# Optimization experiments

Hardware: AMD Instinct MI355X
Metric: run time of the kernel (lower is better)

## Reference

```python
import jax, jax.numpy as jnp
import numpy as np

# norse LIFParameters defaults: tau_syn_inv=200, tau_mem_inv=100, v_leak=0, v_th=1, v_reset=0
DT = 0.001
TAU_SYN_INV = 200.0
TAU_MEM_INV = 100.0
V_TH = 1.0
ALPHA = 100.0  # super-spike surrogate slope

@jax.custom_vjp
def spike(x):
    return (x > 0).astype(x.dtype)

def _spike_fwd(x):
    return (x > 0).astype(x.dtype), x

def _spike_bwd(x, g):
    return (g / (ALPHA * jnp.abs(x) + 1.0) ** 2,)

spike.defvjp(_spike_fwd, _spike_bwd)

def setup_inputs() -> dict:
    key = jax.random.key(0)
    ks = jax.random.split(key, 5)
    T, B, C, FS = 100, 256, 3, 32
    H, D, O, NOUT = 200, 3, 4, 10
    K = H // O
    x = jax.random.normal(ks[0], (T, B, C, FS, FS), dtype=jnp.float32)
    # 3 input channels x 3 dendritic sub-cells, each Linear(FS*FS -> H)
    W_h = jax.random.normal(ks[1], (C, D, H, FS * FS), dtype=jnp.float32) * 0.03
    b_h = jax.random.normal(ks[2], (C, D, H), dtype=jnp.float32) * 0.01
    # 4 output branches, each Linear(K -> 10) feeding a leaky integrator
    W_o = jax.random.normal(ks[3], (O, NOUT, K), dtype=jnp.float32) * 0.1
    b_o = jax.random.normal(ks[4], (O, NOUT), dtype=jnp.float32) * 0.01
    return {"x": x, "W_h": W_h, "b_h": b_h, "W_o": W_o, "b_o": b_o}

def reference(x, W_h, b_h, W_o, b_o):
    T, B = x.shape[0], x.shape[1]
    C, D, H = W_h.shape[0], W_h.shape[1], W_h.shape[2]
    O, NOUT, K = W_o.shape
    xf = x.reshape(T, B, C, -1)  # flatten(1) of each channel slice
    vh0 = jnp.zeros((C, D, B, H), x.dtype)
    ih0 = jnp.zeros((C, D, B, H), x.dtype)
    vo0 = jnp.zeros((O, B, NOUT), x.dtype)
    io0 = jnp.zeros((O, B, NOUT), x.dtype)

    def step(state, x_t):
        vh, ih, vo, io = state
        # hidden dendritic LIF cells (norse lif_feed_forward_step order)
        vh_dec = vh + DT * TAU_MEM_INV * (-vh + ih)  # v_leak = 0
        ih_dec = ih * (1.0 - DT * TAU_SYN_INV)
        zh = spike(vh_dec - V_TH)                    # (C, D, B, H)
        vh_new = (1.0 - zh) * vh_dec                 # v_reset = 0
        inj = jnp.einsum('bci,cdhi->cdbh', x_t, W_h) + b_h[:, :, None, :]
        ih_new = ih_dec + inj
        z = zh.sum(axis=(0, 1))                      # summed dendritic spikes (B, H)
        # output: O contiguous chunks of z -> leaky-integrator readouts
        zs = z.reshape(B, O, K).transpose(1, 0, 2)   # (O, B, K)
        vo_new = vo + DT * TAU_MEM_INV * (-vo + io)
        io_new = io * (1.0 - DT * TAU_SYN_INV) \
                 + jnp.einsum('obk,onk->obn', zs, W_o) + b_o[:, None, :]
        v = vo_new.sum(axis=0)                       # (B, 10)
        return (vh_new, ih_new, vo_new, io_new), v

    _, voltages = jax.lax.scan(step, (vh0, ih0, vo0, io0), xf)
    return voltages  # (T, B, 10)
```

## Files before the change

kernel.cpp:

```cpp
#include <hip/hip_runtime.h>
#include <stdint.h>

#define TOTAL_T 100
#define NB 256
#define NH 200
#define NJ (NB*NH)
#define KDIM 1024
#define NEFF 600
#define NPAD 640
#define NTILES 5
#define KBLKS 32

#define BM 128
#define BN 128
#define AST 1040

#define WCHUNK 4096
#define NWHALF (3 * KBLKS * NTILES * WCHUNK)

typedef _Float16 f16x8 __attribute__((ext_vector_type(8)));
typedef float    f32x4 __attribute__((ext_vector_type(4)));

__global__ __launch_bounds__(256) void presplit_wh(
    const float* __restrict__ Wh, unsigned short* __restrict__ WH,
    unsigned short* __restrict__ WM)
{
    int idx = blockIdx.x * 256 + threadIdx.x;
    if (idx >= 3 * NPAD * KDIM) return;
    int k = idx & (KDIM - 1);
    int n = (idx >> 10) % NPAD;
    int c = idx / (NPAD * KDIM);
    float v = 0.f;
    if (n < NEFF) v = Wh[((size_t)c * NEFF + n) * KDIM + k];
    _Float16 h = (_Float16)v;
    float r = v - (float)h;
    _Float16 m = (_Float16)r;
    int kb = k >> 5, kg = (k >> 3) & 3, kj = k & 7;
    int nt = n >> 7, row = n & 127;
    size_t off = (((size_t)c * KBLKS + kb) * NTILES + nt) * WCHUNK
               + (kg * 128 + row) * 8 + kj;
    WH[off] = __builtin_bit_cast(unsigned short, h);
    WM[off] = __builtin_bit_cast(unsigned short, m);
}

#define SPLIT_A()                                                               \
  {                                                                             \
    _Pragma("unroll")                                                           \
    for (int l = 0; l < 4; ++l) {                                               \
      int row_ = srow + (l << 5);                                               \
      float a0 = av[l].x, a1 = av[l].y, a2 = av[l].z, a3 = av[l].w;             \
      _Float16 h0 = (_Float16)a0, h1 = (_Float16)a1,                            \
               h2 = (_Float16)a2, h3 = (_Float16)a3;                            \
      _Float16 q0 = (_Float16)(a0 - (float)h0), q1 = (_Float16)(a1 - (float)h1),\
               q2 = (_Float16)(a2 - (float)h2), q3 = (_Float16)(a3 - (float)h3);\
      uint32_t hw0 = (uint32_t)__builtin_bit_cast(unsigned short, h0)           \
                   | ((uint32_t)__builtin_bit_cast(unsigned short, h1) << 16);  \
      uint32_t hw1 = (uint32_t)__builtin_bit_cast(unsigned short, h2)           \
                   | ((uint32_t)__builtin_bit_cast(unsigned short, h3) << 16);  \
      uint32_t mw0 = (uint32_t)__builtin_bit_cast(unsigned short, q0)           \
                   | ((uint32_t)__builtin_bit_cast(unsigned short, q1) << 16);  \
      uint32_t mw1 = (uint32_t)__builtin_bit_cast(unsigned short, q2)           \
                   | ((uint32_t)__builtin_bit_cast(unsigned short, q3) << 16);  \
      int off_ = kgw * AST + row_ * 8 + kjw;                                    \
      *reinterpret_cast<uint2*>(&Ah[off_]) = make_uint2(hw0, hw1);              \
      *reinterpret_cast<uint2*>(&Am[off_]) = make_uint2(mw0, mw1);              \
    }                                                                           \
  }

#define GEMM_ITER(KB, BCH, BCM, BNH, BNM)                                       \
  {                                                                             \
    const int kb_ = (KB);                                                       \
    if (kb_ + 1 < KBLKS) {                                                      \
      const unsigned short* nbh_ = bhp + (size_t)(kb_ + 1) * (NTILES * WCHUNK); \
      const unsigned short* nbm_ = bmp + (size_t)(kb_ + 1) * (NTILES * WCHUNK); \
      _Pragma("unroll")                                                         \
      for (int ni = 0; ni < 4; ++ni) {                                          \
        BNH[ni] = *reinterpret_cast<const f16x8*>(nbh_ + bfroff + (ni << 7));   \
        BNM[ni] = *reinterpret_cast<const f16x8*>(nbm_ + bfroff + (ni << 7));   \
      }                                                                         \
      _Pragma("unroll")                                                         \
      for (int l = 0; l < 4; ++l)                                               \
        av[l] = *reinterpret_cast<const float4*>(                               \
            xb + (size_t)(srow + (l << 5)) * 3 * KDIM + ((kb_ + 1) << 5));      \
    }                                                                           \
    f16x8 afh[4], afm[4];                                                       \
    _Pragma("unroll")                                                           \
    for (int mi = 0; mi < 4; ++mi) {                                            \
      int aoff_ = kg * AST + (mbase + (mi << 4) + lrow) * 8;                    \
      afh[mi] = *reinterpret_cast<const f16x8*>(&Ah[aoff_]);                    \
      afm[mi] = *reinterpret_cast<const f16x8*>(&Am[aoff_]);                    \
    }                                                                           \
    asm volatile("s_waitcnt lgkmcnt(0)" ::: "memory");                          \
    __builtin_amdgcn_s_barrier();                                               \
    __builtin_amdgcn_sched_barrier(0);                                          \
    __builtin_amdgcn_s_setprio(1);                                              \
    _Pragma("unroll")                                                           \
    for (int ni = 0; ni < 4; ++ni)                                              \
      _Pragma("unroll")                                                         \
      for (int mi = 0; mi < 4; ++mi) {                                          \
        f32x4 a_ = acc[mi][ni];                                                 \
        a_ = __builtin_amdgcn_mfma_f32_16x16x32_f16(afh[mi], BCH[ni], a_,0,0,0);\
        a_ = __builtin_amdgcn_mfma_f32_16x16x32_f16(afh[mi], BCM[ni], a_,0,0,0);\
        a_ = __builtin_amdgcn_mfma_f32_16x16x32_f16(afm[mi], BCH[ni], a_,0,0,0);\
        acc[mi][ni] = a_;                                                       \
      }                                                                         \
    __builtin_amdgcn_s_setprio(0);                                              \
    __builtin_amdgcn_sched_barrier(0);                                          \
    if (kb_ + 1 < KBLKS) { SPLIT_A(); }                                         \
    asm volatile("s_waitcnt lgkmcnt(0)" ::: "memory");                          \
    __builtin_amdgcn_s_barrier();                                               \
    __builtin_amdgcn_sched_barrier(0);                                          \
  }

__global__ __launch_bounds__(256, 2) void gemm_inj_mfma(
    const float* __restrict__ x,
    const unsigned short* __restrict__ WH,
    const unsigned short* __restrict__ WM,
    const float* __restrict__ bh,
    float* __restrict__ inj,
    int Mc, int MBlk)
{
    __shared__ __align__(16) unsigned short Ah[4 * AST], Am[4 * AST];

    const int tid  = threadIdx.x;
    const int lane = tid & 63;
    const int w    = tid >> 6;
    const int mbase = (w >> 1) * 64;
    const int nbase = (w & 1) * 64;

    const int nblk = gridDim.x;
    const int hwid = blockIdx.x;
    const int xcd  = hwid & 7, jj = hwid >> 3;
    const int q = nblk >> 3, rr = nblk & 7;
    const int L = (xcd < rr ? xcd * (q + 1) : rr * (q + 1) + (xcd - rr) * q) + jj;
    const int c   = L / (NTILES * MBlk);
    const int rem = L - c * (NTILES * MBlk);
    const int mb  = rem / NTILES;
    const int nt  = rem - mb * NTILES;
    const int n0 = nt * BN;
    const int m0 = mb * BM;

    f32x4 acc[4][4];
#pragma unroll
    for (int i = 0; i < 4; ++i)
#pragma unroll
        for (int j = 0; j < 4; ++j) acc[i][j] = (f32x4)0.f;

    const int srow = tid >> 3;
    const int skq  = (tid & 7) << 2;
    const int kgw  = skq >> 3;
    const int kjw  = skq & 7;
    const int kg   = lane >> 4;
    const int lrow = lane & 15;
    const int bfroff = ((kg << 7) + nbase + lrow) << 3;

    const unsigned short* bhp = WH + ((size_t)c * KBLKS * NTILES + nt) * WCHUNK;
    const unsigned short* bmp = WM + ((size_t)c * KBLKS * NTILES + nt) * WCHUNK;
    const float* xb = x + (size_t)m0 * 3 * KDIM + (size_t)c * KDIM + skq;

    f16x8 bAh[4], bAm[4], bBh[4], bBm[4];
    float4 av[4];

#pragma unroll
    for (int ni = 0; ni < 4; ++ni) {
        bAh[ni] = *reinterpret_cast<const f16x8*>(bhp + bfroff + (ni << 7));
        bAm[ni] = *reinterpret_cast<const f16x8*>(bmp + bfroff + (ni << 7));
    }
#pragma unroll
    for (int l = 0; l < 4; ++l)
        av[l] = *reinterpret_cast<const float4*>(xb + (size_t)(srow + (l << 5)) * 3 * KDIM);
    SPLIT_A();
    asm volatile("s_waitcnt lgkmcnt(0)" ::: "memory");
    __builtin_amdgcn_s_barrier();
    __builtin_amdgcn_sched_barrier(0);

    for (int kb2 = 0; kb2 < KBLKS; kb2 += 2) {
        GEMM_ITER(kb2,     bAh, bAm, bBh, bBm);
        GEMM_ITER(kb2 + 1, bBh, bBm, bAh, bAm);
    }

#pragma unroll
    for (int ni = 0; ni < 4; ++ni) {
        int ncol = n0 + nbase + (ni << 4) + lrow;
        if (ncol >= NEFF) continue;
        int d = ncol / 200;
        int h = ncol - d * 200;
        float bias = bh[c * NEFF + ncol];
        size_t obase = (size_t)(c * 3 + d) * Mc;
#pragma unroll
        for (int mi = 0; mi < 4; ++mi) {
            int mrow = m0 + mbase + (mi << 4) + ((lane >> 4) << 2);
#pragma unroll
            for (int r = 0; r < 4; ++r)
                inj[(obase + mrow + r) * NH + h] = acc[mi][ni][r] + bias;
        }
    }
}

__global__ __launch_bounds__(256) void scan_z(
    const float* __restrict__ inj,
    float* __restrict__ z,
    float* __restrict__ vhs, float* __restrict__ ihs,
    int Tc, int first)
{
    int j = blockIdx.x * 256 + threadIdx.x;
    float vh[9], ih[9];
    if (first) {
#pragma unroll
        for (int cd = 0; cd < 9; ++cd) { vh[cd] = 0.f; ih[cd] = 0.f; }
    } else {
#pragma unroll
        for (int cd = 0; cd < 9; ++cd) {
            vh[cd] = vhs[cd * NJ + j];
            ih[cd] = ihs[cd * NJ + j];
        }
    }
    float ivc[9], ivn[9];
#pragma unroll
    for (int cd = 0; cd < 9; ++cd)
        ivc[cd] = inj[(size_t)cd * Tc * NJ + j];
    if (Tc > 1) {
#pragma unroll
        for (int cd = 0; cd < 9; ++cd)
            ivn[cd] = inj[((size_t)cd * Tc + 1) * NJ + j];
    }
    for (int t = 0; t < Tc; ++t) {
        float zs = 0.f;
#pragma unroll
        for (int cd = 0; cd < 9; ++cd) {
            float iv = ivc[cd];
            ivc[cd] = ivn[cd];
            float vd = vh[cd] + 0.1f * (ih[cd] - vh[cd]);
            ih[cd] = 0.8f * ih[cd] + iv;
            if (vd > 1.0f) { zs += 1.f; vh[cd] = 0.f; }
            else           { vh[cd] = vd; }
        }
        z[(size_t)t * NJ + j] = zs;
        if (t + 2 < Tc) {
#pragma unroll
            for (int cd = 0; cd < 9; ++cd)
                ivn[cd] = inj[((size_t)cd * Tc + t + 2) * NJ + j];
        }
    }
#pragma unroll
    for (int cd = 0; cd < 9; ++cd) {
        vhs[cd * NJ + j] = vh[cd];
        ihs[cd * NJ + j] = ih[cd];
    }
}

__global__ __launch_bounds__(256) void readout(
    const float* __restrict__ z,
    const float* __restrict__ Wo,
    const float* __restrict__ bo,
    float* __restrict__ out,
    float* __restrict__ ios, float* __restrict__ vos,
    int t0, int Tc, int first)
{
    const int b = blockIdx.x;
    const int tid = threadIdx.x;
    __shared__ float ush[TOTAL_T][40];
    __shared__ float usum[TOTAL_T][10];
    __shared__ float p9[TOTAL_T + 1], p8[TOTAL_T + 1];
    __shared__ float wsh[2000], bsh[40];
    for (int i = tid; i < 2000; i += 256) wsh[i] = Wo[i];
    if (tid < 40) bsh[tid] = bo[tid];
    if (tid == 0) {
        float a9 = 1.f, a8 = 1.f;
        for (int i = 0; i <= TOTAL_T; ++i) {
            p9[i] = a9; p8[i] = a8; a9 *= 0.9f; a8 *= 0.8f;
        }
    }
    __syncthreads();
    for (int it = tid; it < Tc * 40; it += 256) {
        int s = it / 40, on = it - s * 40;
        int o = on / 10;
        const float* zr = z + (size_t)s * NJ + b * NH + o * 50;
        const float* wr = &wsh[on * 50];
        float dot = bsh[on];
#pragma unroll
        for (int k = 0; k < 50; ++k) dot += zr[k] * wr[k];
        ush[s][on] = dot;
    }
    __syncthreads();
    for (int it = tid; it < Tc * 10; it += 256) {
        int s = it / 10, n = it - s * 10;
        usum[s][n] = ush[s][n] + ush[s][10 + n] + ush[s][20 + n] + ush[s][30 + n];
    }
    __syncthreads();
    for (int it = tid; it < Tc * 10; it += 256) {
        int t = it / 10, n = it - t * 10;
        float a = 0.f;
        for (int s = 0; s <= t; ++s)
            a += (p9[t - s] - p8[t - s]) * usum[s][n];
        if (!first) {
#pragma unroll
            for (int o = 0; o < 4; ++o) {
                int on = o * 10 + n;
                a += p9[t + 1] * vos[b * 40 + on]
                   + (p9[t + 1] - p8[t + 1]) * ios[b * 40 + on];
            }
        }
        out[((size_t)(t0 + t) * NB + b) * 10 + n] = a;
    }
    __syncthreads();
    if (tid < 40) {
        int on = tid;
        float io0 = 0.f, vo0 = 0.f;
        if (!first) { io0 = ios[b * 40 + on]; vo0 = vos[b * 40 + on]; }
        float sio = 0.f, svo = 0.f;
        for (int s = 0; s < Tc; ++s) {
            sio += p8[Tc - 1 - s] * ush[s][on];
            svo += (p9[Tc - 1 - s] - p8[Tc - 1 - s]) * ush[s][on];
        }
        ios[b * 40 + on] = p8[Tc] * io0 + sio;
        vos[b * 40 + on] = p9[Tc] * vo0 + (p9[Tc] - p8[Tc]) * io0 + svo;
    }
}

extern "C" void kernel_launch(void* const* d_in, const int* in_sizes, int n_in,
                              void* d_out, int out_size, void* d_ws, size_t ws_size,
                              hipStream_t stream) {
    (void)in_sizes; (void)n_in; (void)out_size;
    const float* x  = (const float*)d_in[0];
    const float* Wh = (const float*)d_in[1];
    const float* bh = (const float*)d_in[2];
    const float* Wo = (const float*)d_in[3];
    const float* bo = (const float*)d_in[4];
    float* out = (float*)d_out;

    float* vhs  = (float*)d_ws;
    float* ihs  = vhs + 9 * NJ;
    float* ios  = ihs + 9 * NJ;
    float* vos  = ios + NB * 40;
    unsigned short* WHl = (unsigned short*)(vos + NB * 40);
    unsigned short* WMl = WHl + NWHALF;
    float* inj  = (float*)(WMl + NWHALF);

    size_t fixed = ((size_t)9 * NJ * 2 + (size_t)NB * 40 * 2) * 4
                 + (size_t)NWHALF * 2 * 2;
    size_t per_t = (size_t)NB * (9 * NH * 4 + NH * 4);
    int Tc = 1;
    for (int t = TOTAL_T; t >= 1; --t) {
        if (fixed + (size_t)t * per_t <= ws_size) { Tc = t; break; }
    }

    presplit_wh<<<(3 * NPAD * KDIM + 255) / 256, 256, 0, stream>>>(Wh, WHl, WMl);

    for (int t0 = 0; t0 < TOTAL_T; t0 += Tc) {
        int tc = (TOTAL_T - t0 < Tc) ? (TOTAL_T - t0) : Tc;
        int Mc = tc * NB;
        int MBlk = Mc / BM;
        float* zbuf = inj + (size_t)9 * Mc * NH;
        gemm_inj_mfma<<<NTILES * MBlk * 3, 256, 0, stream>>>(
            x + (size_t)t0 * NB * 3 * KDIM, WHl, WMl, bh, inj, Mc, MBlk);
        scan_z<<<NJ / 256, 256, 0, stream>>>(inj, zbuf, vhs, ihs, tc, t0 == 0);
        readout<<<NB, 256, 0, stream>>>(
            zbuf, Wo, bo, out, ios, vos, t0, tc, t0 == 0);
    }
}
```

Before: 450.6 us.

## Load A fragments directly into registers, dropping LDS staging and barriers

The A tile is no longer staged through shared memory. Each lane now loads the eight fp32 values of its own MFMA fragment straight from global memory and splits them into fp16 high and low parts in registers. This removes the LDS writes and reads and both workgroup barriers per K step, with the A and B loads for the next K block software-pipelined around the MFMA cluster. The block-index decomposition also changes so blocks sharing the same N tile run consecutively, which should improve B-weight cache reuse. In exchange, the two waves covering the same rows issue duplicate global loads of x, and there is less slack to hide global latency than with the LDS buffer.

```diff
diff --git a/kernel.cpp b/kernel.cpp
--- a/kernel.cpp
+++ b/kernel.cpp
@@ -13,7 +13,6 @@
 
 #define BM 128
 #define BN 128
-#define AST 1040
 
 #define WCHUNK 4096
 #define NWHALF (3 * KBLKS * NTILES * WCHUNK)
@@ -43,73 +42,56 @@
     WM[off] = __builtin_bit_cast(unsigned short, m);
 }
 
-#define SPLIT_A()                                                               \
+
+#define LOAD_AB(KB, BH_, BM_)                                                   \
   {                                                                             \
     _Pragma("unroll")                                                           \
-    for (int l = 0; l < 4; ++l) {                                               \
-      int row_ = srow + (l << 5);                                               \
-      float a0 = av[l].x, a1 = av[l].y, a2 = av[l].z, a3 = av[l].w;             \
-      _Float16 h0 = (_Float16)a0, h1 = (_Float16)a1,                            \
-               h2 = (_Float16)a2, h3 = (_Float16)a3;                            \
-      _Float16 q0 = (_Float16)(a0 - (float)h0), q1 = (_Float16)(a1 - (float)h1),\
-               q2 = (_Float16)(a2 - (float)h2), q3 = (_Float16)(a3 - (float)h3);\
-      uint32_t hw0 = (uint32_t)__builtin_bit_cast(unsigned short, h0)           \
-                   | ((uint32_t)__builtin_bit_cast(unsigned short, h1) << 16);  \
-      uint32_t hw1 = (uint32_t)__builtin_bit_cast(unsigned short, h2)           \
-                   | ((uint32_t)__builtin_bit_cast(unsigned short, h3) << 16);  \
-      uint32_t mw0 = (uint32_t)__builtin_bit_cast(unsigned short, q0)           \
-                   | ((uint32_t)__builtin_bit_cast(unsigned short, q1) << 16);  \
-      uint32_t mw1 = (uint32_t)__builtin_bit_cast(unsigned short, q2)           \
-                   | ((uint32_t)__builtin_bit_cast(unsigned short, q3) << 16);  \
-      int off_ = kgw * AST + row_ * 8 + kjw;                                    \
-      *reinterpret_cast<uint2*>(&Ah[off_]) = make_uint2(hw0, hw1);              \
-      *reinterpret_cast<uint2*>(&Am[off_]) = make_uint2(mw0, mw1);              \
+    for (int mi = 0; mi < 4; ++mi) {                                            \
+      avn[2 * mi]     = *reinterpret_cast<const float4*>(ap[mi] + ((KB) << 5));     \
+      avn[2 * mi + 1] = *reinterpret_cast<const float4*>(ap[mi] + ((KB) << 5) + 4); \
+    }                                                                           \
+    const unsigned short* nb_ = bhp + (size_t)(KB) * (NTILES * WCHUNK);         \
+    const unsigned short* nm_ = bmp + (size_t)(KB) * (NTILES * WCHUNK);         \
+    _Pragma("unroll")                                                           \
+    for (int ni = 0; ni < 4; ++ni) {                                            \
+      BH_[ni] = *reinterpret_cast<const f16x8*>(nb_ + (ni << 7));               \
+      BM_[ni] = *reinterpret_cast<const f16x8*>(nm_ + (ni << 7));               \
     }                                                                           \
   }
 
-#define GEMM_ITER(KB, BCH, BCM, BNH, BNM)                                       \
+#define SPLIT_AV()                                                              \
   {                                                                             \
-    const int kb_ = (KB);                                                       \
-    if (kb_ + 1 < KBLKS) {                                                      \
-      const unsigned short* nbh_ = bhp + (size_t)(kb_ + 1) * (NTILES * WCHUNK); \
-      const unsigned short* nbm_ = bmp + (size_t)(kb_ + 1) * (NTILES * WCHUNK); \
-      _Pragma("unroll")                                                         \
-      for (int ni = 0; ni < 4; ++ni) {                                          \
-        BNH[ni] = *reinterpret_cast<const f16x8*>(nbh_ + bfroff + (ni << 7));   \
-        BNM[ni] = *reinterpret_cast<const f16x8*>(nbm_ + bfroff + (ni << 7));   \
-      }                                                                         \
-      _Pragma("unroll")                                                         \
-      for (int l = 0; l < 4; ++l)                                               \
-        av[l] = *reinterpret_cast<const float4*>(                               \
-            xb + (size_t)(srow + (l << 5)) * 3 * KDIM + ((kb_ + 1) << 5));      \
-    }                                                                           \
-    f16x8 afh[4], afm[4];                                                       \
     _Pragma("unroll")                                                           \
     for (int mi = 0; mi < 4; ++mi) {                                            \
-      int aoff_ = kg * AST + (mbase + (mi << 4) + lrow) * 8;                    \
-      afh[mi] = *reinterpret_cast<const f16x8*>(&Ah[aoff_]);                    \
-      afm[mi] = *reinterpret_cast<const f16x8*>(&Am[aoff_]);                    \
+      float xr[8];                                                              \
+      xr[0] = avn[2 * mi].x;     xr[1] = avn[2 * mi].y;                         \
+      xr[2] = avn[2 * mi].z;     xr[3] = avn[2 * mi].w;                         \
+      xr[4] = avn[2 * mi + 1].x; xr[5] = avn[2 * mi + 1].y;                     \
+      xr[6] = avn[2 * mi + 1].z; xr[7] = avn[2 * mi + 1].w;                     \
+      _Pragma("unroll")                                                         \
+      for (int j2 = 0; j2 < 8; ++j2) {                                          \
+        _Float16 hv = (_Float16)xr[j2];                                         \
+        _Float16 mv = (_Float16)(xr[j2] - (float)hv);                           \
+        afh[mi][j2] = hv;                                                       \
+        afm[mi][j2] = mv;                                                       \
+      }                                                                         \
     }                                                                           \
-    asm volatile("s_waitcnt lgkmcnt(0)" ::: "memory");                          \
-    __builtin_amdgcn_s_barrier();                                               \
-    __builtin_amdgcn_sched_barrier(0);                                          \
+  }
+
+#define MFMA_CL(BH_, BM_)                                                       \
+  {                                                                             \
     __builtin_amdgcn_s_setprio(1);                                              \
     _Pragma("unroll")                                                           \
     for (int ni = 0; ni < 4; ++ni)                                              \
       _Pragma("unroll")                                                         \
       for (int mi = 0; mi < 4; ++mi) {                                          \
         f32x4 a_ = acc[mi][ni];                                                 \
-        a_ = __builtin_amdgcn_mfma_f32_16x16x32_f16(afh[mi], BCH[ni], a_,0,0,0);\
-        a_ = __builtin_amdgcn_mfma_f32_16x16x32_f16(afh[mi], BCM[ni], a_,0,0,0);\
-        a_ = __builtin_amdgcn_mfma_f32_16x16x32_f16(afm[mi], BCH[ni], a_,0,0,0);\
+        a_ = __builtin_amdgcn_mfma_f32_16x16x32_f16(afh[mi], BH_[ni], a_,0,0,0);\
+        a_ = __builtin_amdgcn_mfma_f32_16x16x32_f16(afh[mi], BM_[ni], a_,0,0,0);\
+        a_ = __builtin_amdgcn_mfma_f32_16x16x32_f16(afm[mi], BH_[ni], a_,0,0,0);\
         acc[mi][ni] = a_;                                                       \
       }                                                                         \
     __builtin_amdgcn_s_setprio(0);                                              \
-    __builtin_amdgcn_sched_barrier(0);                                          \
-    if (kb_ + 1 < KBLKS) { SPLIT_A(); }                                         \
-    asm volatile("s_waitcnt lgkmcnt(0)" ::: "memory");                          \
-    __builtin_amdgcn_s_barrier();                                               \
-    __builtin_amdgcn_sched_barrier(0);                                          \
   }
 
 __global__ __launch_bounds__(256, 2) void gemm_inj_mfma(
@@ -120,8 +102,6 @@
     float* __restrict__ inj,
     int Mc, int MBlk)
 {
-    __shared__ __align__(16) unsigned short Ah[4 * AST], Am[4 * AST];
-
     const int tid  = threadIdx.x;
     const int lane = tid & 63;
     const int w    = tid >> 6;
@@ -135,49 +115,56 @@
     const int L = (xcd < rr ? xcd * (q + 1) : rr * (q + 1) + (xcd - rr) * q) + jj;
     const int c   = L / (NTILES * MBlk);
     const int rem = L - c * (NTILES * MBlk);
-    const int mb  = rem / NTILES;
-    const int nt  = rem - mb * NTILES;
+    const int nt  = rem / MBlk;
+    const int mb  = rem - nt * MBlk;
     const int n0 = nt * BN;
     const int m0 = mb * BM;
 
-    f32x4 acc[4][4];
-#pragma unroll
-    for (int i = 0; i < 4; ++i)
-#pragma unroll
-        for (int j = 0; j < 4; ++j) acc[i][j] = (f32x4)0.f;
-
-    const int srow = tid >> 3;
-    const int skq  = (tid & 7) << 2;
-    const int kgw  = skq >> 3;
-    const int kjw  = skq & 7;
     const int kg   = lane >> 4;
     const int lrow = lane & 15;
     const int bfroff = ((kg << 7) + nbase + lrow) << 3;
 
-    const unsigned short* bhp = WH + ((size_t)c * KBLKS * NTILES + nt) * WCHUNK;
-    const unsigned short* bmp = WM + ((size_t)c * KBLKS * NTILES + nt) * WCHUNK;
-    const float* xb = x + (size_t)m0 * 3 * KDIM + (size_t)c * KDIM + skq;
-
-    f16x8 bAh[4], bAm[4], bBh[4], bBm[4];
-    float4 av[4];
-
-#pragma unroll
-    for (int ni = 0; ni < 4; ++ni) {
-        bAh[ni] = *reinterpret_cast<const f16x8*>(bhp + bfroff + (ni << 7));
-        bAm[ni] = *reinterpret_cast<const f16x8*>(bmp + bfroff + (ni << 7));
-    }
-#pragma unroll
-    for (int l = 0; l < 4; ++l)
-        av[l] = *reinterpret_cast<const float4*>(xb + (size_t)(srow + (l << 5)) * 3 * KDIM);
-    SPLIT_A();
-    asm volatile("s_waitcnt lgkmcnt(0)" ::: "memory");
-    __builtin_amdgcn_s_barrier();
+    f32x4 acc[4][4];
+#pragma unroll
+    for (int i = 0; i < 4; ++i)
+#pragma unroll
+        for (int j = 0; j < 4; ++j) acc[i][j] = (f32x4)0.f;
+
+    const float* ap[4];
+#pragma unroll
+    for (int mi = 0; mi < 4; ++mi)
+        ap[mi] = x + (size_t)(m0 + mbase + (mi << 4) + lrow) * (3 * KDIM)
+               + (size_t)c * KDIM + (kg << 3);
+
+    const unsigned short* bhp = WH + ((size_t)c * KBLKS * NTILES + nt) * WCHUNK + bfroff;
+    const unsigned short* bmp = WM + ((size_t)c * KBLKS * NTILES + nt) * WCHUNK + bfroff;
+
+    float4 avn[8];
+    f16x8 b0h[4], b0m[4], b1h[4], b1m[4];
+    f16x8 afh[4], afm[4];
+
+    LOAD_AB(0, b0h, b0m);
+    SPLIT_AV();
+
+    for (int kb2 = 0; kb2 < KBLKS - 2; kb2 += 2) {
+        LOAD_AB(kb2 + 1, b1h, b1m);
+        __builtin_amdgcn_sched_barrier(0);
+        MFMA_CL(b0h, b0m);
+        __builtin_amdgcn_sched_barrier(0);
+        SPLIT_AV();
+        LOAD_AB(kb2 + 2, b0h, b0m);
+        __builtin_amdgcn_sched_barrier(0);
+        MFMA_CL(b1h, b1m);
+        __builtin_amdgcn_sched_barrier(0);
+        SPLIT_AV();
+    }
+    LOAD_AB(KBLKS - 1, b1h, b1m);
     __builtin_amdgcn_sched_barrier(0);
-
-    for (int kb2 = 0; kb2 < KBLKS; kb2 += 2) {
-        GEMM_ITER(kb2,     bAh, bAm, bBh, bBm);
-        GEMM_ITER(kb2 + 1, bBh, bBm, bAh, bAm);
-    }
+    MFMA_CL(b0h, b0m);
+    __builtin_amdgcn_sched_barrier(0);
+    SPLIT_AV();
+    __builtin_amdgcn_sched_barrier(0);
+    MFMA_CL(b1h, b1m);
 
 #pragma unroll
     for (int ni = 0; ni < 4; ++ni) {
```

Result: slower. 682.0 us (+51.4%).

## Stage B operand through triple-buffered LDS via async global_load_lds

Applied to the files above, without the earlier changes.

The precomputed fp16 hi/lo weight tiles are no longer loaded from global memory straight into registers per wave. They are now copied with global_load_lds into a three-deep LDS ring buffer, prefetched two K-blocks ahead, and read into fragments from LDS. The goal is to hide global-memory latency behind the MFMA work and to stop each wave from fetching its own B fragments separately. The cost is 48KB of extra LDS per block, which could limit occupancy, plus hand-tuned vmcnt waits whose counts must match the issued loads exactly. The K loop is reorganised into a 3-way unrolled main loop plus a peeled two-block epilogue.

```diff
diff --git a/kernel.cpp b/kernel.cpp
--- a/kernel.cpp
+++ b/kernel.cpp
@@ -20,6 +20,8 @@
 
 typedef _Float16 f16x8 __attribute__((ext_vector_type(8)));
 typedef float    f32x4 __attribute__((ext_vector_type(4)));
+typedef __attribute__((address_space(3))) uint32_t as3_u32;
+typedef __attribute__((address_space(1))) uint32_t as1_u32;
 
 __global__ __launch_bounds__(256) void presplit_wh(
     const float* __restrict__ Wh, unsigned short* __restrict__ WH,
@@ -43,16 +45,41 @@
     WM[off] = __builtin_bit_cast(unsigned short, m);
 }
 
+
+#define LOAD_A(KB)                                                              \
+  {                                                                             \
+    _Pragma("unroll")                                                           \
+    for (int l = 0; l < 4; ++l)                                                 \
+      avn[l] = *reinterpret_cast<const float4*>(                                \
+          xb + (size_t)(srow + (l << 5)) * 3 * KDIM + ((KB) << 5));             \
+  }
+
+#define DMA_B(KB, BUF)                                                          \
+  {                                                                             \
+    const unsigned short* nbh_ = bhp + (size_t)(KB) * (NTILES * WCHUNK);        \
+    const unsigned short* nbm_ = bmp + (size_t)(KB) * (NTILES * WCHUNK);        \
+    _Pragma("unroll")                                                           \
+    for (int i = 0; i < 2; ++i) {                                               \
+      int seg = (i << 2) + w;                                                   \
+      __builtin_amdgcn_global_load_lds(                                         \
+          (const as1_u32*)(nbh_ + ((seg << 6) + lane) * 8),                     \
+          (as3_u32*)&Bh[BUF][seg << 9], 16, 0, 0);                              \
+      __builtin_amdgcn_global_load_lds(                                         \
+          (const as1_u32*)(nbm_ + ((seg << 6) + lane) * 8),                     \
+          (as3_u32*)&Bm[BUF][seg << 9], 16, 0, 0);                              \
+    }                                                                           \
+  }
+
 #define SPLIT_A()                                                               \
   {                                                                             \
     _Pragma("unroll")                                                           \
     for (int l = 0; l < 4; ++l) {                                               \
       int row_ = srow + (l << 5);                                               \
-      float a0 = av[l].x, a1 = av[l].y, a2 = av[l].z, a3 = av[l].w;             \
+      float a0 = avn[l].x, a1 = avn[l].y, a2 = avn[l].z, a3 = avn[l].w;         \
       _Float16 h0 = (_Float16)a0, h1 = (_Float16)a1,                            \
                h2 = (_Float16)a2, h3 = (_Float16)a3;                            \
-      _Float16 q0 = (_Float16)(a0 - (float)h0), q1 = (_Float16)(a1 - (float)h1),\
-               q2 = (_Float16)(a2 - (float)h2), q3 = (_Float16)(a3 - (float)h3);\
+      _Float16 q0 = (_Float16)(a0 - (float)h0), q1 = (_Float16)(a1 - (float)h1);\
+      _Float16 q2 = (_Float16)(a2 - (float)h2), q3 = (_Float16)(a3 - (float)h3);\
       uint32_t hw0 = (uint32_t)__builtin_bit_cast(unsigned short, h0)           \
                    | ((uint32_t)__builtin_bit_cast(unsigned short, h1) << 16);  \
       uint32_t hw1 = (uint32_t)__builtin_bit_cast(unsigned short, h2)           \
@@ -67,46 +94,51 @@
     }                                                                           \
   }
 
-#define GEMM_ITER(KB, BCH, BCM, BNH, BNM)                                       \
-  {                                                                             \
-    const int kb_ = (KB);                                                       \
-    if (kb_ + 1 < KBLKS) {                                                      \
-      const unsigned short* nbh_ = bhp + (size_t)(kb_ + 1) * (NTILES * WCHUNK); \
-      const unsigned short* nbm_ = bmp + (size_t)(kb_ + 1) * (NTILES * WCHUNK); \
-      _Pragma("unroll")                                                         \
-      for (int ni = 0; ni < 4; ++ni) {                                          \
-        BNH[ni] = *reinterpret_cast<const f16x8*>(nbh_ + bfroff + (ni << 7));   \
-        BNM[ni] = *reinterpret_cast<const f16x8*>(nbm_ + bfroff + (ni << 7));   \
-      }                                                                         \
-      _Pragma("unroll")                                                         \
-      for (int l = 0; l < 4; ++l)                                               \
-        av[l] = *reinterpret_cast<const float4*>(                               \
-            xb + (size_t)(srow + (l << 5)) * 3 * KDIM + ((kb_ + 1) << 5));      \
-    }                                                                           \
-    f16x8 afh[4], afm[4];                                                       \
+#define FRAGS(RBUF)                                                             \
+  {                                                                             \
     _Pragma("unroll")                                                           \
     for (int mi = 0; mi < 4; ++mi) {                                            \
       int aoff_ = kg * AST + (mbase + (mi << 4) + lrow) * 8;                    \
       afh[mi] = *reinterpret_cast<const f16x8*>(&Ah[aoff_]);                    \
       afm[mi] = *reinterpret_cast<const f16x8*>(&Am[aoff_]);                    \
     }                                                                           \
-    asm volatile("s_waitcnt lgkmcnt(0)" ::: "memory");                          \
-    __builtin_amdgcn_s_barrier();                                               \
-    __builtin_amdgcn_sched_barrier(0);                                          \
+    _Pragma("unroll")                                                           \
+    for (int ni = 0; ni < 4; ++ni) {                                            \
+      int boff_ = ((kg << 7) + nbase + (ni << 4) + lrow) << 3;                  \
+      bfh[ni] = *reinterpret_cast<const f16x8*>(&Bh[RBUF][boff_]);              \
+      bfm[ni] = *reinterpret_cast<const f16x8*>(&Bm[RBUF][boff_]);              \
+    }                                                                           \
+  }
+
+#define MFMA_CL()                                                               \
+  {                                                                             \
     __builtin_amdgcn_s_setprio(1);                                              \
     _Pragma("unroll")                                                           \
     for (int ni = 0; ni < 4; ++ni)                                              \
       _Pragma("unroll")                                                         \
       for (int mi = 0; mi < 4; ++mi) {                                          \
         f32x4 a_ = acc[mi][ni];                                                 \
-        a_ = __builtin_amdgcn_mfma_f32_16x16x32_f16(afh[mi], BCH[ni], a_,0,0,0);\
-        a_ = __builtin_amdgcn_mfma_f32_16x16x32_f16(afh[mi], BCM[ni], a_,0,0,0);\
-        a_ = __builtin_amdgcn_mfma_f32_16x16x32_f16(afm[mi], BCH[ni], a_,0,0,0);\
+        a_ = __builtin_amdgcn_mfma_f32_16x16x32_f16(afh[mi], bfh[ni], a_,0,0,0);\
+        a_ = __builtin_amdgcn_mfma_f32_16x16x32_f16(afh[mi], bfm[ni], a_,0,0,0);\
+        a_ = __builtin_amdgcn_mfma_f32_16x16x32_f16(afm[mi], bfh[ni], a_,0,0,0);\
         acc[mi][ni] = a_;                                                       \
       }                                                                         \
     __builtin_amdgcn_s_setprio(0);                                              \
+  }
+
+#define G_ITER(KB, RBUF, IBUF)                                                  \
+  {                                                                             \
+    LOAD_A((KB) + 1);                                                           \
+    DMA_B((KB) + 2, IBUF);                                                      \
+    FRAGS(RBUF);                                                                \
+    asm volatile("s_waitcnt lgkmcnt(0)" ::: "memory");                          \
+    __builtin_amdgcn_s_barrier();                                               \
     __builtin_amdgcn_sched_barrier(0);                                          \
-    if (kb_ + 1 < KBLKS) { SPLIT_A(); }                                         \
+    MFMA_CL();                                                                  \
+    __builtin_amdgcn_sched_barrier(0);                                          \
+    asm volatile("s_waitcnt vmcnt(4)" ::: "memory");                            \
+    __builtin_amdgcn_sched_barrier(0);                                          \
+    SPLIT_A();                                                                  \
     asm volatile("s_waitcnt lgkmcnt(0)" ::: "memory");                          \
     __builtin_amdgcn_s_barrier();                                               \
     __builtin_amdgcn_sched_barrier(0);                                          \
@@ -121,6 +153,7 @@
     int Mc, int MBlk)
 {
     __shared__ __align__(16) unsigned short Ah[4 * AST], Am[4 * AST];
+    __shared__ __align__(16) unsigned short Bh[3][4096], Bm[3][4096];
 
     const int tid  = threadIdx.x;
     const int lane = tid & 63;
@@ -152,32 +185,47 @@
     const int kjw  = skq & 7;
     const int kg   = lane >> 4;
     const int lrow = lane & 15;
-    const int bfroff = ((kg << 7) + nbase + lrow) << 3;
 
     const unsigned short* bhp = WH + ((size_t)c * KBLKS * NTILES + nt) * WCHUNK;
     const unsigned short* bmp = WM + ((size_t)c * KBLKS * NTILES + nt) * WCHUNK;
     const float* xb = x + (size_t)m0 * 3 * KDIM + (size_t)c * KDIM + skq;
 
-    f16x8 bAh[4], bAm[4], bBh[4], bBm[4];
-    float4 av[4];
-
-#pragma unroll
-    for (int ni = 0; ni < 4; ++ni) {
-        bAh[ni] = *reinterpret_cast<const f16x8*>(bhp + bfroff + (ni << 7));
-        bAm[ni] = *reinterpret_cast<const f16x8*>(bmp + bfroff + (ni << 7));
-    }
-#pragma unroll
-    for (int l = 0; l < 4; ++l)
-        av[l] = *reinterpret_cast<const float4*>(xb + (size_t)(srow + (l << 5)) * 3 * KDIM);
+    float4 avn[4];
+    f16x8 afh[4], afm[4], bfh[4], bfm[4];
+
+    LOAD_A(0);
+    DMA_B(0, 0);
+    DMA_B(1, 1);
+    asm volatile("s_waitcnt vmcnt(8)" ::: "memory");
+    __builtin_amdgcn_sched_barrier(0);
+    SPLIT_A();
+    asm volatile("s_waitcnt vmcnt(4)" ::: "memory");
+    asm volatile("s_waitcnt lgkmcnt(0)" ::: "memory");
+    __builtin_amdgcn_s_barrier();
+    __builtin_amdgcn_sched_barrier(0);
+
+    for (int kb3 = 0; kb3 < 30; kb3 += 3) {
+        G_ITER(kb3 + 0, 0, 2);
+        G_ITER(kb3 + 1, 1, 0);
+        G_ITER(kb3 + 2, 2, 1);
+    }
+    LOAD_A(31);
+    FRAGS(0);
+    asm volatile("s_waitcnt lgkmcnt(0)" ::: "memory");
+    __builtin_amdgcn_s_barrier();
+    __builtin_amdgcn_sched_barrier(0);
+    MFMA_CL();
+    __builtin_amdgcn_sched_barrier(0);
+    asm volatile("s_waitcnt vmcnt(0)" ::: "memory");
+    __builtin_amdgcn_sched_barrier(0);
     SPLIT_A();
     asm volatile("s_waitcnt lgkmcnt(0)" ::: "memory");
     __builtin_amdgcn_s_barrier();
     __builtin_amdgcn_sched_barrier(0);
-
-    for (int kb2 = 0; kb2 < KBLKS; kb2 += 2) {
-        GEMM_ITER(kb2,     bAh, bAm, bBh, bBm);
-        GEMM_ITER(kb2 + 1, bBh, bBm, bAh, bAm);
-    }
+    FRAGS(1);
+    asm volatile("s_waitcnt lgkmcnt(0)" ::: "memory");
+    __builtin_amdgcn_sched_barrier(0);
+    MFMA_CL();
 
 #pragma unroll
     for (int ni = 0; ni < 4; ++ni) {
```

Result: slower. 549.5 us (+21.9%).
